# Kernel optimization log

Measured on AMD Instinct MI355X. Metric: run time of the kernel, lower is better.

The kernel has to match this reference:

```python
import jax, jax.numpy as jnp
import numpy as np

B, S, D_MODEL, D_HEAD = 4, 4096, 512, 64


def setup_inputs() -> dict:
    key = jax.random.key(0)
    ks = jax.random.split(key, 9)
    s = 1.0 / np.sqrt(D_MODEL)
    return {
        "q_in": jax.random.normal(ks[0], (B, S, D_MODEL), jnp.float32),
        "k_in": jax.random.normal(ks[1], (B, S, D_MODEL), jnp.float32),
        "v_in": jax.random.normal(ks[2], (B, S, D_MODEL), jnp.float32),
        "Wq": jax.random.normal(ks[3], (D_HEAD, D_MODEL), jnp.float32) * s,
        "bq": jax.random.normal(ks[4], (D_HEAD,), jnp.float32) * s,
        "Wk": jax.random.normal(ks[5], (D_HEAD, D_MODEL), jnp.float32) * s,
        "bk": jax.random.normal(ks[6], (D_HEAD,), jnp.float32) * s,
        "Wv": jax.random.normal(ks[7], (D_HEAD, D_MODEL), jnp.float32) * s,
        "bv": jax.random.normal(ks[8], (D_HEAD,), jnp.float32) * s,
    }


def reference(q_in, k_in, v_in, Wq, bq, Wk, bk, Wv, bv):
    # Linear projections (torch nn.Linear: x @ W.T + b)
    q = jnp.einsum("bsd,hd->bsh", q_in, Wq) + bq  # [B,S,Dh]
    k = jnp.einsum("bsd,hd->bsh", k_in, Wk) + bk
    v = jnp.einsum("bsd,hd->bsh", v_in, Wv) + bv
    # Causal mask: -inf strictly above diagonal (generate_attention_mask, triu(1))
    sk = k.shape[1]
    mask = jnp.triu(jnp.full((q.shape[1], sk), -jnp.inf, dtype=q.dtype), k=1)
    scores = jnp.einsum("bqh,bkh->bqk", q, k) / jnp.sqrt(jnp.asarray(q.shape[-1], q.dtype))
    attn = jax.nn.softmax(scores + mask, axis=-1)  # [B,S,S]
    return jnp.einsum("bqk,bkh->bqh", attn, v)
```

## Files before the change

### kernel.cpp

```cpp
#include <hip/hip_runtime.h>
#include <hip/hip_bf16.h>

#define B_ 4
#define S_ 4096
#define DM 512
#define DH 64

#define NEG_BIG (-3.0e38f)
#define MCLAMP  (-1.0e30f)

typedef __attribute__((ext_vector_type(8))) short short8b;
typedef __attribute__((ext_vector_type(4))) float f32x4;

__device__ __forceinline__ f32x4 MFMA16(short8b a, short8b b, f32x4 c) {
    return __builtin_amdgcn_mfma_f32_16x16x32_bf16(a, b, c, 0, 0, 0);
}

__device__ __forceinline__ float bf2f(unsigned short u) {
    unsigned int x = ((unsigned int)u) << 16;
    float f;
    __builtin_memcpy(&f, &x, 4);
    return f;
}
__device__ __forceinline__ unsigned short f2bf_rne(float f) {
    unsigned int u = __float_as_uint(f);
    u += 0x7FFFu + ((u >> 16) & 1u);
    return (unsigned short)(u >> 16);
}
__device__ __forceinline__ unsigned int pk2(unsigned short a, unsigned short b) {
    return (unsigned int)a | ((unsigned int)b << 16);
}

__device__ __forceinline__ void gload16(const void* gp, void* lp) {
    __builtin_amdgcn_global_load_lds(
        (const __attribute__((address_space(1))) void*)gp,
        (__attribute__((address_space(3))) void*)lp, 16, 0, 0);
}

__global__ void detect_kernel(const unsigned short* __restrict__ u,
                              int* __restrict__ flag) {
    __shared__ int cnt;
    if (threadIdx.x == 0) cnt = 0;
    __syncthreads();
    int w = 0;
    #pragma unroll
    for (int k = 0; k < 8; ++k) {
        unsigned short x = u[threadIdx.x * 8 + k];
        int e = (x >> 7) & 0xFF;
        if (e >= 135 || (e > 0 && e <= 95)) ++w;
    }
    atomicAdd(&cnt, w);
    __syncthreads();
    if (threadIdx.x == 0) *flag = (cnt > 64) ? 1 : 0;
}

#define PM 64
#define PK 64

__global__ __launch_bounds__(256) void proj_kernel(
    const void* __restrict__ xq, const void* __restrict__ xk,
    const void* __restrict__ xv,
    const void* __restrict__ Wq, const void* __restrict__ Wk,
    const void* __restrict__ Wv,
    const void* __restrict__ bq, const void* __restrict__ bk,
    const void* __restrict__ bv,
    unsigned short* __restrict__ Qhp, unsigned short* __restrict__ Qlp,
    unsigned short* __restrict__ Khp, unsigned short* __restrict__ Klp,
    unsigned short* __restrict__ Vthp, unsigned short* __restrict__ Vtlp,
    const int* __restrict__ flag)
{
    const int which = blockIdx.y;
    const void* x    = (which == 0) ? xq : (which == 1) ? xk : xv;
    const void* W    = (which == 0) ? Wq : (which == 1) ? Wk : Wv;
    const void* bias = (which == 0) ? bq : (which == 1) ? bk : bv;

    const bool f32 = (*flag != 0);
    const int row0 = blockIdx.x * PM;
    const int t    = threadIdx.x;
    const int lane = t & 63;
    const int w    = t >> 6;
    const int l15  = lane & 15;
    const int l4   = lane >> 4;

    __shared__ __align__(16) char sm[32768];

    const int srow = t >> 2;
    const int sseg = t & 3;
    const int swz  = (srow & 7) << 4;

    f32x4 acc[4];
    #pragma unroll
    for (int n = 0; n < 4; ++n) acc[n] = f32x4{0.f, 0.f, 0.f, 0.f};

    #pragma unroll 1
    for (int kc = 0; kc < DM / PK; ++kc) {
        const int k0 = kc * PK;
        __syncthreads();

        if (f32) {
            #pragma unroll
            for (int m = 0; m < 2; ++m) {
                const float* p = (m == 0)
                    ? (const float*)x + (size_t)(row0 + srow) * DM + k0 + sseg * 16
                    : (const float*)W + (size_t)srow * DM + k0 + sseg * 16;
                float v[16];
                #pragma unroll
                for (int j = 0; j < 4; ++j) {
                    float4 f = *reinterpret_cast<const float4*>(p + j * 4);
                    v[j * 4 + 0] = f.x; v[j * 4 + 1] = f.y;
                    v[j * 4 + 2] = f.z; v[j * 4 + 3] = f.w;
                }
                unsigned short hh[16], ll[16];
                #pragma unroll
                for (int j = 0; j < 16; ++j) {
                    unsigned short hb = f2bf_rne(v[j]);
                    hh[j] = hb;
                    ll[j] = f2bf_rne(v[j] - bf2f(hb));
                }
                char* dh = sm + m * 16384 + srow * 128;
                char* dl = dh + 8192;
                #pragma unroll
                for (int g = 0; g < 2; ++g) {
                    const int off = (sseg * 32 + g * 16) ^ swz;
                    uint4 hu, lu;
                    hu.x = pk2(hh[g*8+0], hh[g*8+1]); hu.y = pk2(hh[g*8+2], hh[g*8+3]);
                    hu.z = pk2(hh[g*8+4], hh[g*8+5]); hu.w = pk2(hh[g*8+6], hh[g*8+7]);
                    lu.x = pk2(ll[g*8+0], ll[g*8+1]); lu.y = pk2(ll[g*8+2], ll[g*8+3]);
                    lu.z = pk2(ll[g*8+4], ll[g*8+5]); lu.w = pk2(ll[g*8+6], ll[g*8+7]);
                    *reinterpret_cast<uint4*>(dh + off) = hu;
                    *reinterpret_cast<uint4*>(dl + off) = lu;
                }
            }
        } else {
            const uint4 z = {0u, 0u, 0u, 0u};
            #pragma unroll
            for (int m = 0; m < 2; ++m) {
                const unsigned short* p = (m == 0)
                    ? (const unsigned short*)x + (size_t)(row0 + srow) * DM + k0 + sseg * 16
                    : (const unsigned short*)W + (size_t)srow * DM + k0 + sseg * 16;
                char* dh = sm + m * 16384 + srow * 128;
                char* dl = dh + 8192;
                #pragma unroll
                for (int g = 0; g < 2; ++g) {
                    uint4 hv = *reinterpret_cast<const uint4*>(p + g * 8);
                    const int off = (sseg * 32 + g * 16) ^ swz;
                    *reinterpret_cast<uint4*>(dh + off) = hv;
                    *reinterpret_cast<uint4*>(dl + off) = z;
                }
            }
        }
        __syncthreads();

        const int arow = w * 16 + l15;
        short8b xh[2], xl[2];
        #pragma unroll
        for (int ks = 0; ks < 2; ++ks) {
            const int off = arow * 128 + ((ks * 64 + l4 * 16) ^ ((arow & 7) << 4));
            xh[ks] = *reinterpret_cast<const short8b*>(sm + off);
            xl[ks] = *reinterpret_cast<const short8b*>(sm + 8192 + off);
        }
        #pragma unroll
        for (int n = 0; n < 4; ++n) {
            #pragma unroll
            for (int ks = 0; ks < 2; ++ks) {
                const int brow = n * 16 + l15;
                const int off = brow * 128 + ((ks * 64 + l4 * 16) ^ ((brow & 7) << 4));
                short8b wh = *reinterpret_cast<const short8b*>(sm + 16384 + off);
                short8b wl = *reinterpret_cast<const short8b*>(sm + 24576 + off);
                acc[n] = MFMA16(xh[ks], wl, acc[n]);
                acc[n] = MFMA16(xl[ks], wh, acc[n]);
                acc[n] = MFMA16(xh[ks], wh, acc[n]);
            }
        }
    }

    __syncthreads();
    float* C = reinterpret_cast<float*>(sm);
    #pragma unroll
    for (int n = 0; n < 4; ++n)
        #pragma unroll
        for (int r = 0; r < 4; ++r)
            C[(w * 16 + l4 * 4 + r) * 66 + n * 16 + l15] = acc[n][r];
    __syncthreads();

    if (which < 2) {
        unsigned short* ph = (which == 0) ? Qhp : Khp;
        unsigned short* pl = (which == 0) ? Qlp : Klp;
        const float scale = (which == 0) ? 0.125f : 1.0f;
        const int r_  = t >> 2;
        const int c0_ = (t & 3) * 16;
        unsigned short hh[16], ll[16];
        #pragma unroll
        for (int j = 0; j < 16; ++j) {
            const float bv_ = f32 ? ((const float*)bias)[c0_ + j]
                                  : bf2f(((const unsigned short*)bias)[c0_ + j]);
            const float v = (C[r_ * 66 + c0_ + j] + bv_) * scale;
            unsigned short hb = f2bf_rne(v);
            hh[j] = hb;
            ll[j] = f2bf_rne(v - bf2f(hb));
        }
        const size_t off = (size_t)(row0 + r_) * DH + c0_;
        #pragma unroll
        for (int g = 0; g < 2; ++g) {
            uint4 hu, lu;
            hu.x = pk2(hh[g*8+0], hh[g*8+1]); hu.y = pk2(hh[g*8+2], hh[g*8+3]);
            hu.z = pk2(hh[g*8+4], hh[g*8+5]); hu.w = pk2(hh[g*8+6], hh[g*8+7]);
            lu.x = pk2(ll[g*8+0], ll[g*8+1]); lu.y = pk2(ll[g*8+2], ll[g*8+3]);
            lu.z = pk2(ll[g*8+4], ll[g*8+5]); lu.w = pk2(ll[g*8+6], ll[g*8+7]);
            *reinterpret_cast<uint4*>(ph + off + g * 8) = hu;
            *reinterpret_cast<uint4*>(pl + off + g * 8) = lu;
        }
    } else {
        const int c_ = t & 63;
        const int rb = (t >> 6) * 16;
        const int bb = row0 >> 12;
        const int s0 = row0 & (S_ - 1);
        const float bv_ = f32 ? ((const float*)bias)[c_]
                              : bf2f(((const unsigned short*)bias)[c_]);
        unsigned short hh[16], ll[16];
        #pragma unroll
        for (int i = 0; i < 16; ++i) {
            const float v = C[(rb + i) * 66 + c_] + bv_;
            unsigned short hb = f2bf_rne(v);
            hh[i] = hb;
            ll[i] = f2bf_rne(v - bf2f(hb));
        }
        const size_t off = (size_t)(bb * 64 + c_) * S_ + s0 + rb;
        #pragma unroll
        for (int g = 0; g < 2; ++g) {
            uint4 hu, lu;
            hu.x = pk2(hh[g*8+0], hh[g*8+1]); hu.y = pk2(hh[g*8+2], hh[g*8+3]);
            hu.z = pk2(hh[g*8+4], hh[g*8+5]); hu.w = pk2(hh[g*8+6], hh[g*8+7]);
            lu.x = pk2(ll[g*8+0], ll[g*8+1]); lu.y = pk2(ll[g*8+2], ll[g*8+3]);
            lu.z = pk2(ll[g*8+4], ll[g*8+5]); lu.w = pk2(ll[g*8+6], ll[g*8+7]);
            *reinterpret_cast<uint4*>(Vthp + off + g * 8) = hu;
            *reinterpret_cast<uint4*>(Vtlp + off + g * 8) = lu;
        }
    }
}

__global__ __launch_bounds__(512, 2) void flash_kernel(
    const unsigned short* __restrict__ Qh, const unsigned short* __restrict__ Ql,
    const unsigned short* __restrict__ Kh, const unsigned short* __restrict__ Kl,
    const unsigned short* __restrict__ Vth, const unsigned short* __restrict__ Vtl,
    void* __restrict__ out, const int* __restrict__ flag)
{
    const int pair = blockIdx.x;
    const int b    = blockIdx.y;
    const int t    = threadIdx.x;
    const int lane = t & 63;
    const int w    = t >> 6;
    const int qh   = w & 1;
    const int kh   = w >> 1;
    const int l15  = lane & 15;
    const int l4   = lane >> 4;

    __shared__ __align__(16) char smem[8192 + 2 * 65536];
    __shared__ float Mg[4][32];
    __shared__ float Lg[4][32];
    __shared__ float Ltot[32];

    const size_t bS = (size_t)b * S_;
    const bool f32o = (*flag != 0);

    const int qp   = t >> 8;
    const int qrow = (t & 255) >> 3;
    const int qsg  = t & 7;

    const int klaneoff = ((lane >> 3) << 7) +
                         ((((lane & 7) << 4)) ^ ((lane >> 3) << 4));
    const int vrl = lane >> 4;
    const int voff0 = (vrl << 13) + ((((lane & 15) << 4)) ^ (vrl << 4));
    const int voff1 = (vrl << 13) + ((((lane & 15) << 4)) ^ ((4 + vrl) << 4));

    const char* Khb = (const char*)Kh + bS * 128;
    const char* Klb = (const char*)Kl + bS * 128;
    const char* Vhb = (const char*)Vth + (size_t)b * 64 * 8192;
    const char* Vlb = (const char*)Vtl + (size_t)b * 64 * 8192;

    auto issue_tile = [&](int kt, int bsel) {
        char* buf = smem + 8192 + bsel * 65536;
        if (w < 4) {
            #pragma unroll
            for (int j = 0; j < 8; ++j) {
                const int c2  = w * 8 + j;
                const int p   = c2 >> 4;
                const int ckp = c2 & 15;
                const char* g = (p ? Klb : Khb) +
                                (size_t)kt * 16384 + ckp * 1024 + klaneoff;
                gload16(g, buf + p * 16384 + ckp * 1024);
            }
        } else {
            #pragma unroll
            for (int j = 0; j < 8; ++j) {
                const int c2  = (w - 4) * 8 + j;
                const int p   = c2 >> 4;
                const int cvp = c2 & 15;
                const int vo  = (cvp & 1) ? voff1 : voff0;
                const char* g = (p ? Vlb : Vhb) +
                                (size_t)cvp * 32768 + (size_t)kt * 256 + vo;
                gload16(g, buf + 32768 + p * 16384 + cvp * 1024);
            }
        }
    };

    #pragma unroll 1
    for (int hf = 0; hf < 2; ++hf) {
        const int qt = hf ? (127 - pair) : pair;
        const int q0 = qt << 5;
        const int nk = (qt >> 2) + 1;

        __syncthreads();

        {
            const unsigned short* src = qp ? Ql : Qh;
            uint4 v = *reinterpret_cast<const uint4*>(
                src + (bS + q0 + qrow) * 64 + qsg * 8);
            const int off = qp * 4096 + qrow * 128 +
                            ((qsg * 16) ^ ((qrow & 7) << 4));
            *reinterpret_cast<uint4*>(smem + off) = v;
        }
        issue_tile(0, 0);
        __syncthreads();

        short8b qf[2][2];
        #pragma unroll
        for (int p = 0; p < 2; ++p)
            #pragma unroll
            for (int ks = 0; ks < 2; ++ks) {
                const int row = qh * 16 + l15;
                const int off = p * 4096 + row * 128 +
                                ((ks * 64 + l4 * 16) ^ ((row & 7) << 4));
                qf[p][ks] = *reinterpret_cast<const short8b*>(smem + off);
            }
        __syncthreads();

        f32x4 of[4];
        of[0] = f32x4{0.f, 0.f, 0.f, 0.f};
        of[1] = f32x4{0.f, 0.f, 0.f, 0.f};
        of[2] = f32x4{0.f, 0.f, 0.f, 0.f};
        of[3] = f32x4{0.f, 0.f, 0.f, 0.f};
        float mrun[4], lrun[4];
        #pragma unroll
        for (int r = 0; r < 4; ++r) { mrun[r] = NEG_BIG; lrun[r] = 0.f; }

        #pragma unroll 1
        for (int kt = 0; kt < nk; ++kt) {
            const int bsel = kt & 1;
            if (kt + 1 < nk) issue_tile(kt + 1, bsel ^ 1);

            const char* kb = smem + 8192 + bsel * 65536;
            const char* vb = kb + 32768;

            f32x4 sc[2];
            #pragma unroll
            for (int ct = 0; ct < 2; ++ct) {
                f32x4 a = f32x4{0.f, 0.f, 0.f, 0.f};
                #pragma unroll
                for (int ks = 0; ks < 2; ++ks) {
                    const int row = kh * 32 + ct * 16 + l15;
                    const int off = row * 128 +
                                    ((ks * 64 + l4 * 16) ^ ((row & 7) << 4));
                    short8b bh = *reinterpret_cast<const short8b*>(kb + off);
                    short8b bl = *reinterpret_cast<const short8b*>(kb + 16384 + off);
                    a = MFMA16(qf[1][ks], bh, a);
                    a = MFMA16(qf[0][ks], bl, a);
                    a = MFMA16(qf[0][ks], bh, a);
                }
                sc[ct] = a;
            }

            if (kt == nk - 1) {
                #pragma unroll
                for (int ct = 0; ct < 2; ++ct) {
                    const int col = kt * 128 + kh * 32 + ct * 16 + l15;
                    #pragma unroll
                    for (int r = 0; r < 4; ++r) {
                        const int row = q0 + qh * 16 + l4 * 4 + r;
                        if (col > row) sc[ct][r] = NEG_BIG;
                    }
                }
            }

            float pm[4];
            #pragma unroll
            for (int r = 0; r < 4; ++r) pm[r] = fmaxf(sc[0][r], sc[1][r]);
            #pragma unroll
            for (int s = 1; s < 16; s <<= 1)
                #pragma unroll
                for (int r = 0; r < 4; ++r)
                    pm[r] = fmaxf(pm[r], __shfl_xor(pm[r], s));

            float alpha[4], ps[4];
            #pragma unroll
            for (int r = 0; r < 4; ++r) {
                const float mn = fmaxf(fmaxf(mrun[r], pm[r]), MCLAMP);
                alpha[r] = __expf(mrun[r] - mn);
                mrun[r] = mn;
                sc[0][r] = __expf(sc[0][r] - mn);
                sc[1][r] = __expf(sc[1][r] - mn);
                ps[r] = sc[0][r] + sc[1][r];
            }
            #pragma unroll
            for (int s = 1; s < 16; s <<= 1)
                #pragma unroll
                for (int r = 0; r < 4; ++r) ps[r] += __shfl_xor(ps[r], s);
            #pragma unroll
            for (int r = 0; r < 4; ++r) lrun[r] = lrun[r] * alpha[r] + ps[r];
            #pragma unroll
            for (int c = 0; c < 4; ++c)
                #pragma unroll
                for (int r = 0; r < 4; ++r) of[c][r] *= alpha[r];

            #pragma unroll
            for (int ct = 0; ct < 2; ++ct)
                #pragma unroll
                for (int r = 0; r < 4; ++r) {
                    const int row = qh * 16 + l4 * 4 + r;
                    const int col = kh * 32 + ct * 16 + l15;
                    const int off = row * 256 + ((col * 2) ^ ((row & 7) << 4));
                    *reinterpret_cast<unsigned short*>(smem + off) =
                        f2bf_rne(sc[ct][r]);
                }
            asm volatile("s_waitcnt lgkmcnt(0)" ::: "memory");
            __builtin_amdgcn_sched_barrier(0);

            short8b pf;
            {
                const int row = qh * 16 + l15;
                const int off = row * 256 + ((kh * 64 + l4 * 16) ^ ((row & 7) << 4));
                pf = *reinterpret_cast<const short8b*>(smem + off);
            }
            #pragma unroll
            for (int ct = 0; ct < 4; ++ct) {
                const int vr = ct * 16 + l15;
                const int voff = vr * 256 +
                                 ((kh * 64 + l4 * 16) ^ ((vr & 7) << 4));
                short8b vh = *reinterpret_cast<const short8b*>(vb + voff);
                short8b vl = *reinterpret_cast<const short8b*>(vb + 16384 + voff);
                of[ct] = MFMA16(pf, vl, of[ct]);
                of[ct] = MFMA16(pf, vh, of[ct]);
            }

            __syncthreads();
        }

        if (l15 == 0) {
            #pragma unroll
            for (int r = 0; r < 4; ++r) {
                const int row = qh * 16 + l4 * 4 + r;
                Mg[kh][row] = mrun[r];
                Lg[kh][row] = lrun[r];
            }
        }
        __syncthreads();

        float* Op = reinterpret_cast<float*>(smem + 8192);
        #pragma unroll
        for (int r = 0; r < 4; ++r) {
            const int row = qh * 16 + l4 * 4 + r;
            const float M = fmaxf(fmaxf(Mg[0][row], Mg[1][row]),
                                  fmaxf(Mg[2][row], Mg[3][row]));
            const float L = Lg[0][row] * __expf(Mg[0][row] - M)
                          + Lg[1][row] * __expf(Mg[1][row] - M)
                          + Lg[2][row] * __expf(Mg[2][row] - M)
                          + Lg[3][row] * __expf(Mg[3][row] - M);
            const float al = __expf(mrun[r] - M);
            #pragma unroll
            for (int c = 0; c < 4; ++c)
                Op[kh * 2048 + row * 64 + c * 16 + l15] = of[c][r] * al;
            if (kh == 0 && l15 == 0) Ltot[row] = L;
        }
        __syncthreads();

        {
            const int row = t >> 4;
            const int d0  = (t & 15) << 2;
            float4 s = {0.f, 0.f, 0.f, 0.f};
            #pragma unroll
            for (int g = 0; g < 4; ++g) {
                float4 v = *reinterpret_cast<const float4*>(
                    Op + g * 2048 + row * 64 + d0);
                s.x += v.x; s.y += v.y; s.z += v.z; s.w += v.w;
            }
            const float inv = 1.0f / Ltot[row];
            const size_t oi = (bS + q0 + row) * 64 + d0;
            if (f32o) {
                float4 o;
                o.x = s.x * inv; o.y = s.y * inv;
                o.z = s.z * inv; o.w = s.w * inv;
                *reinterpret_cast<float4*>((float*)out + oi) = o;
            } else {
                ushort4 o;
                o.x = f2bf_rne(s.x * inv);
                o.y = f2bf_rne(s.y * inv);
                o.z = f2bf_rne(s.z * inv);
                o.w = f2bf_rne(s.w * inv);
                *reinterpret_cast<ushort4*>((unsigned short*)out + oi) = o;
            }
        }
    }
}

extern "C" void kernel_launch(void* const* d_in, const int* in_sizes, int n_in,
                              void* d_out, int out_size, void* d_ws, size_t ws_size,
                              hipStream_t stream) {
    const size_t NP = (size_t)B_ * S_ * DH;
    unsigned short* Qhp  = (unsigned short*)d_ws;
    unsigned short* Qlp  = Qhp + NP;
    unsigned short* Khp  = Qhp + 2 * NP;
    unsigned short* Klp  = Qhp + 3 * NP;
    unsigned short* Vthp = Qhp + 4 * NP;
    unsigned short* Vtlp = Qhp + 5 * NP;
    int* flag = (int*)(Qhp + 6 * NP);

    detect_kernel<<<1, 256, 0, stream>>>((const unsigned short*)d_in[0], flag);

    proj_kernel<<<dim3(B_ * S_ / PM, 3), 256, 0, stream>>>(
        d_in[0], d_in[1], d_in[2],
        d_in[3], d_in[5], d_in[7],
        d_in[4], d_in[6], d_in[8],
        Qhp, Qlp, Khp, Klp, Vthp, Vtlp, flag);

    flash_kernel<<<dim3(64, B_), 512, 0, stream>>>(
        Qhp, Qlp, Khp, Klp, Vthp, Vtlp, d_out, flag);
}
```

Measured before the change: 220.0 us.

## Fuse detect, projection and flash attention into one cooperative persistent kernel

```diff
diff --git a/kernel.cpp b/kernel.cpp
--- a/kernel.cpp
+++ b/kernel.cpp
@@ -1,5 +1,8 @@
 #include <hip/hip_runtime.h>
 #include <hip/hip_bf16.h>
+#include <hip/hip_cooperative_groups.h>
+
+namespace cg = cooperative_groups;
 
 #define B_ 4
 #define S_ 4096
@@ -37,27 +40,7 @@
         (__attribute__((address_space(3))) void*)lp, 16, 0, 0);
 }
 
-__global__ void detect_kernel(const unsigned short* __restrict__ u,
-                              int* __restrict__ flag) {
-    __shared__ int cnt;
-    if (threadIdx.x == 0) cnt = 0;
-    __syncthreads();
-    int w = 0;
-    #pragma unroll
-    for (int k = 0; k < 8; ++k) {
-        unsigned short x = u[threadIdx.x * 8 + k];
-        int e = (x >> 7) & 0xFF;
-        if (e >= 135 || (e > 0 && e <= 95)) ++w;
-    }
-    atomicAdd(&cnt, w);
-    __syncthreads();
-    if (threadIdx.x == 0) *flag = (cnt > 64) ? 1 : 0;
-}
-
-#define PM 64
-#define PK 64
-
-__global__ __launch_bounds__(256) void proj_kernel(
+__global__ __launch_bounds__(512, 1) void fused_kernel(
     const void* __restrict__ xq, const void* __restrict__ xk,
     const void* __restrict__ xv,
     const void* __restrict__ Wq, const void* __restrict__ Wk,
@@ -67,436 +50,442 @@
     unsigned short* __restrict__ Qhp, unsigned short* __restrict__ Qlp,
     unsigned short* __restrict__ Khp, unsigned short* __restrict__ Klp,
     unsigned short* __restrict__ Vthp, unsigned short* __restrict__ Vtlp,
-    const int* __restrict__ flag)
+    void* __restrict__ out)
 {
-    const int which = blockIdx.y;
-    const void* x    = (which == 0) ? xq : (which == 1) ? xk : xv;
-    const void* W    = (which == 0) ? Wq : (which == 1) ? Wk : Wv;
-    const void* bias = (which == 0) ? bq : (which == 1) ? bk : bv;
-
-    const bool f32 = (*flag != 0);
-    const int row0 = blockIdx.x * PM;
+    const int blk  = blockIdx.x;
     const int t    = threadIdx.x;
     const int lane = t & 63;
     const int w    = t >> 6;
     const int l15  = lane & 15;
     const int l4   = lane >> 4;
 
-    __shared__ __align__(16) char sm[32768];
-
-    const int srow = t >> 2;
-    const int sseg = t & 3;
-    const int swz  = (srow & 7) << 4;
-
-    f32x4 acc[4];
-    #pragma unroll
-    for (int n = 0; n < 4; ++n) acc[n] = f32x4{0.f, 0.f, 0.f, 0.f};
-
-    #pragma unroll 1
-    for (int kc = 0; kc < DM / PK; ++kc) {
-        const int k0 = kc * PK;
-        __syncthreads();
-
-        if (f32) {
-            #pragma unroll
-            for (int m = 0; m < 2; ++m) {
-                const float* p = (m == 0)
-                    ? (const float*)x + (size_t)(row0 + srow) * DM + k0 + sseg * 16
-                    : (const float*)W + (size_t)srow * DM + k0 + sseg * 16;
-                float v[16];
-                #pragma unroll
-                for (int j = 0; j < 4; ++j) {
-                    float4 f = *reinterpret_cast<const float4*>(p + j * 4);
-                    v[j * 4 + 0] = f.x; v[j * 4 + 1] = f.y;
-                    v[j * 4 + 2] = f.z; v[j * 4 + 3] = f.w;
-                }
-                unsigned short hh[16], ll[16];
-                #pragma unroll
-                for (int j = 0; j < 16; ++j) {
-                    unsigned short hb = f2bf_rne(v[j]);
-                    hh[j] = hb;
-                    ll[j] = f2bf_rne(v[j] - bf2f(hb));
-                }
-                char* dh = sm + m * 16384 + srow * 128;
-                char* dl = dh + 8192;
-                #pragma unroll
-                for (int g = 0; g < 2; ++g) {
-                    const int off = (sseg * 32 + g * 16) ^ swz;
-                    uint4 hu, lu;
-                    hu.x = pk2(hh[g*8+0], hh[g*8+1]); hu.y = pk2(hh[g*8+2], hh[g*8+3]);
-                    hu.z = pk2(hh[g*8+4], hh[g*8+5]); hu.w = pk2(hh[g*8+6], hh[g*8+7]);
-                    lu.x = pk2(ll[g*8+0], ll[g*8+1]); lu.y = pk2(ll[g*8+2], ll[g*8+3]);
-                    lu.z = pk2(ll[g*8+4], ll[g*8+5]); lu.w = pk2(ll[g*8+6], ll[g*8+7]);
-                    *reinterpret_cast<uint4*>(dh + off) = hu;
-                    *reinterpret_cast<uint4*>(dl + off) = lu;
-                }
-            }
-        } else {
-            const uint4 z = {0u, 0u, 0u, 0u};
-            #pragma unroll
-            for (int m = 0; m < 2; ++m) {
-                const unsigned short* p = (m == 0)
-                    ? (const unsigned short*)x + (size_t)(row0 + srow) * DM + k0 + sseg * 16
-                    : (const unsigned short*)W + (size_t)srow * DM + k0 + sseg * 16;
-                char* dh = sm + m * 16384 + srow * 128;
-                char* dl = dh + 8192;
-                #pragma unroll
-                for (int g = 0; g < 2; ++g) {
-                    uint4 hv = *reinterpret_cast<const uint4*>(p + g * 8);
-                    const int off = (sseg * 32 + g * 16) ^ swz;
-                    *reinterpret_cast<uint4*>(dh + off) = hv;
-                    *reinterpret_cast<uint4*>(dl + off) = z;
-                }
-            }
-        }
-        __syncthreads();
-
-        const int arow = w * 16 + l15;
-        short8b xh[2], xl[2];
-        #pragma unroll
-        for (int ks = 0; ks < 2; ++ks) {
-            const int off = arow * 128 + ((ks * 64 + l4 * 16) ^ ((arow & 7) << 4));
-            xh[ks] = *reinterpret_cast<const short8b*>(sm + off);
-            xl[ks] = *reinterpret_cast<const short8b*>(sm + 8192 + off);
-        }
-        #pragma unroll
-        for (int n = 0; n < 4; ++n) {
-            #pragma unroll
-            for (int ks = 0; ks < 2; ++ks) {
-                const int brow = n * 16 + l15;
-                const int off = brow * 128 + ((ks * 64 + l4 * 16) ^ ((brow & 7) << 4));
-                short8b wh = *reinterpret_cast<const short8b*>(sm + 16384 + off);
-                short8b wl = *reinterpret_cast<const short8b*>(sm + 24576 + off);
-                acc[n] = MFMA16(xh[ks], wl, acc[n]);
-                acc[n] = MFMA16(xl[ks], wh, acc[n]);
-                acc[n] = MFMA16(xh[ks], wh, acc[n]);
-            }
-        }
-    }
-
-    __syncthreads();
-    float* C = reinterpret_cast<float*>(sm);
-    #pragma unroll
-    for (int n = 0; n < 4; ++n)
-        #pragma unroll
-        for (int r = 0; r < 4; ++r)
-            C[(w * 16 + l4 * 4 + r) * 66 + n * 16 + l15] = acc[n][r];
-    __syncthreads();
-
-    if (which < 2) {
-        unsigned short* ph = (which == 0) ? Qhp : Khp;
-        unsigned short* pl = (which == 0) ? Qlp : Klp;
-        const float scale = (which == 0) ? 0.125f : 1.0f;
-        const int r_  = t >> 2;
-        const int c0_ = (t & 3) * 16;
-        unsigned short hh[16], ll[16];
-        #pragma unroll
-        for (int j = 0; j < 16; ++j) {
-            const float bv_ = f32 ? ((const float*)bias)[c0_ + j]
-                                  : bf2f(((const unsigned short*)bias)[c0_ + j]);
-            const float v = (C[r_ * 66 + c0_ + j] + bv_) * scale;
-            unsigned short hb = f2bf_rne(v);
-            hh[j] = hb;
-            ll[j] = f2bf_rne(v - bf2f(hb));
-        }
-        const size_t off = (size_t)(row0 + r_) * DH + c0_;
-        #pragma unroll
-        for (int g = 0; g < 2; ++g) {
-            uint4 hu, lu;
-            hu.x = pk2(hh[g*8+0], hh[g*8+1]); hu.y = pk2(hh[g*8+2], hh[g*8+3]);
-            hu.z = pk2(hh[g*8+4], hh[g*8+5]); hu.w = pk2(hh[g*8+6], hh[g*8+7]);
-            lu.x = pk2(ll[g*8+0], ll[g*8+1]); lu.y = pk2(ll[g*8+2], ll[g*8+3]);
-            lu.z = pk2(ll[g*8+4], ll[g*8+5]); lu.w = pk2(ll[g*8+6], ll[g*8+7]);
-            *reinterpret_cast<uint4*>(ph + off + g * 8) = hu;
-            *reinterpret_cast<uint4*>(pl + off + g * 8) = lu;
-        }
-    } else {
-        const int c_ = t & 63;
-        const int rb = (t >> 6) * 16;
-        const int bb = row0 >> 12;
-        const int s0 = row0 & (S_ - 1);
-        const float bv_ = f32 ? ((const float*)bias)[c_]
-                              : bf2f(((const unsigned short*)bias)[c_]);
-        unsigned short hh[16], ll[16];
-        #pragma unroll
-        for (int i = 0; i < 16; ++i) {
-            const float v = C[(rb + i) * 66 + c_] + bv_;
-            unsigned short hb = f2bf_rne(v);
-            hh[i] = hb;
-            ll[i] = f2bf_rne(v - bf2f(hb));
-        }
-        const size_t off = (size_t)(bb * 64 + c_) * S_ + s0 + rb;
-        #pragma unroll
-        for (int g = 0; g < 2; ++g) {
-            uint4 hu, lu;
-            hu.x = pk2(hh[g*8+0], hh[g*8+1]); hu.y = pk2(hh[g*8+2], hh[g*8+3]);
-            hu.z = pk2(hh[g*8+4], hh[g*8+5]); hu.w = pk2(hh[g*8+6], hh[g*8+7]);
-            lu.x = pk2(ll[g*8+0], ll[g*8+1]); lu.y = pk2(ll[g*8+2], ll[g*8+3]);
-            lu.z = pk2(ll[g*8+4], ll[g*8+5]); lu.w = pk2(ll[g*8+6], ll[g*8+7]);
-            *reinterpret_cast<uint4*>(Vthp + off + g * 8) = hu;
-            *reinterpret_cast<uint4*>(Vtlp + off + g * 8) = lu;
-        }
-    }
-}
-
-__global__ __launch_bounds__(512, 2) void flash_kernel(
-    const unsigned short* __restrict__ Qh, const unsigned short* __restrict__ Ql,
-    const unsigned short* __restrict__ Kh, const unsigned short* __restrict__ Kl,
-    const unsigned short* __restrict__ Vth, const unsigned short* __restrict__ Vtl,
-    void* __restrict__ out, const int* __restrict__ flag)
-{
-    const int pair = blockIdx.x;
-    const int b    = blockIdx.y;
-    const int t    = threadIdx.x;
-    const int lane = t & 63;
-    const int w    = t >> 6;
-    const int qh   = w & 1;
-    const int kh   = w >> 1;
-    const int l15  = lane & 15;
-    const int l4   = lane >> 4;
-
     __shared__ __align__(16) char smem[8192 + 2 * 65536];
     __shared__ float Mg[4][32];
     __shared__ float Lg[4][32];
     __shared__ float Ltot[32];
-
-    const size_t bS = (size_t)b * S_;
-    const bool f32o = (*flag != 0);
-
-    const int qp   = t >> 8;
-    const int qrow = (t & 255) >> 3;
-    const int qsg  = t & 7;
-
-    const int klaneoff = ((lane >> 3) << 7) +
-                         ((((lane & 7) << 4)) ^ ((lane >> 3) << 4));
-    const int vrl = lane >> 4;
-    const int voff0 = (vrl << 13) + ((((lane & 15) << 4)) ^ (vrl << 4));
-    const int voff1 = (vrl << 13) + ((((lane & 15) << 4)) ^ ((4 + vrl) << 4));
-
-    const char* Khb = (const char*)Kh + bS * 128;
-    const char* Klb = (const char*)Kl + bS * 128;
-    const char* Vhb = (const char*)Vth + (size_t)b * 64 * 8192;
-    const char* Vlb = (const char*)Vtl + (size_t)b * 64 * 8192;
-
-    auto issue_tile = [&](int kt, int bsel) {
-        char* buf = smem + 8192 + bsel * 65536;
-        if (w < 4) {
+    __shared__ int sdet;
+
+    if (t == 0) sdet = 0;
+    __syncthreads();
+    if (t < 256) {
+        const unsigned short* u = (const unsigned short*)xq;
+        int cnt = 0;
+        #pragma unroll
+        for (int k = 0; k < 8; ++k) {
+            unsigned short x = u[t * 8 + k];
+            int e = (x >> 7) & 0xFF;
+            if (e >= 135 || (e > 0 && e <= 95)) ++cnt;
+        }
+        atomicAdd(&sdet, cnt);
+    }
+    __syncthreads();
+    const bool f32 = (sdet > 64);
+
+    {
+        const int row0 = blk * 64;
+        const int m    = t >> 8;
+        const int tt   = t & 255;
+        const int srow = tt >> 2;
+        const int sseg = tt & 3;
+        const int swz  = (srow & 7) << 4;
+        const int rq   = (w & 3) * 16;
+        const int nb   = (w >> 2) * 2;
+        const int arow = rq + l15;
+
+        #pragma unroll 1
+        for (int which = 0; which < 3; ++which) {
+            const void* x    = (which == 0) ? xq : (which == 1) ? xk : xv;
+            const void* W    = (which == 0) ? Wq : (which == 1) ? Wk : Wv;
+            const void* bias = (which == 0) ? bq : (which == 1) ? bk : bv;
+
+            f32x4 acc[2];
+            acc[0] = f32x4{0.f, 0.f, 0.f, 0.f};
+            acc[1] = f32x4{0.f, 0.f, 0.f, 0.f};
+
+            #pragma unroll 1
+            for (int kc = 0; kc < DM / 64; ++kc) {
+                const int k0 = kc * 64;
+                __syncthreads();
+
+                if (f32) {
+                    const float* p = (m == 0)
+                        ? (const float*)x + (size_t)(row0 + srow) * DM + k0 + sseg * 16
+                        : (const float*)W + (size_t)srow * DM + k0 + sseg * 16;
+                    float v[16];
+                    #pragma unroll
+                    for (int j = 0; j < 4; ++j) {
+                        float4 f = *reinterpret_cast<const float4*>(p + j * 4);
+                        v[j*4+0] = f.x; v[j*4+1] = f.y;
+                        v[j*4+2] = f.z; v[j*4+3] = f.w;
+                    }
+                    unsigned short hh[16], ll[16];
+                    #pragma unroll
+                    for (int j = 0; j < 16; ++j) {
+                        unsigned short hb = f2bf_rne(v[j]);
+                        hh[j] = hb;
+                        ll[j] = f2bf_rne(v[j] - bf2f(hb));
+                    }
+                    char* dh = smem + m * 16384 + srow * 128;
+                    char* dl = dh + 8192;
+                    #pragma unroll
+                    for (int g = 0; g < 2; ++g) {
+                        const int off = (sseg * 32 + g * 16) ^ swz;
+                        uint4 hu, lu;
+                        hu.x = pk2(hh[g*8+0], hh[g*8+1]); hu.y = pk2(hh[g*8+2], hh[g*8+3]);
+                        hu.z = pk2(hh[g*8+4], hh[g*8+5]); hu.w = pk2(hh[g*8+6], hh[g*8+7]);
+                        lu.x = pk2(ll[g*8+0], ll[g*8+1]); lu.y = pk2(ll[g*8+2], ll[g*8+3]);
+                        lu.z = pk2(ll[g*8+4], ll[g*8+5]); lu.w = pk2(ll[g*8+6], ll[g*8+7]);
+                        *reinterpret_cast<uint4*>(dh + off) = hu;
+                        *reinterpret_cast<uint4*>(dl + off) = lu;
+                    }
+                } else {
+                    const unsigned short* p = (m == 0)
+                        ? (const unsigned short*)x + (size_t)(row0 + srow) * DM + k0 + sseg * 16
+                        : (const unsigned short*)W + (size_t)srow * DM + k0 + sseg * 16;
+                    char* dh = smem + m * 16384 + srow * 128;
+                    char* dl = dh + 8192;
+                    const uint4 z = {0u, 0u, 0u, 0u};
+                    #pragma unroll
+                    for (int g = 0; g < 2; ++g) {
+                        uint4 hv = *reinterpret_cast<const uint4*>(p + g * 8);
+                        const int off = (sseg * 32 + g * 16) ^ swz;
+                        *reinterpret_cast<uint4*>(dh + off) = hv;
+                        *reinterpret_cast<uint4*>(dl + off) = z;
+                    }
+                }
+                __syncthreads();
+
+                short8b xh[2], xl[2];
+                #pragma unroll
+                for (int ks = 0; ks < 2; ++ks) {
+                    const int off = arow * 128 + ((ks * 64 + l4 * 16) ^ ((arow & 7) << 4));
+                    xh[ks] = *reinterpret_cast<const short8b*>(smem + off);
+                    xl[ks] = *reinterpret_cast<const short8b*>(smem + 8192 + off);
+                }
+                #pragma unroll
+                for (int n2 = 0; n2 < 2; ++n2) {
+                    const int brow = (nb + n2) * 16 + l15;
+                    #pragma unroll
+                    for (int ks = 0; ks < 2; ++ks) {
+                        const int off = brow * 128 + ((ks * 64 + l4 * 16) ^ ((brow & 7) << 4));
+                        short8b wh = *reinterpret_cast<const short8b*>(smem + 16384 + off);
+                        short8b wl = *reinterpret_cast<const short8b*>(smem + 24576 + off);
+                        acc[n2] = MFMA16(xh[ks], wl, acc[n2]);
+                        acc[n2] = MFMA16(xl[ks], wh, acc[n2]);
+                        acc[n2] = MFMA16(xh[ks], wh, acc[n2]);
+                    }
+                }
+            }
+
+            __syncthreads();
+            float* C = reinterpret_cast<float*>(smem + 32768);
             #pragma unroll
-            for (int j = 0; j < 8; ++j) {
-                const int c2  = w * 8 + j;
-                const int p   = c2 >> 4;
-                const int ckp = c2 & 15;
-                const char* g = (p ? Klb : Khb) +
-                                (size_t)kt * 16384 + ckp * 1024 + klaneoff;
-                gload16(g, buf + p * 16384 + ckp * 1024);
-            }
-        } else {
+            for (int n2 = 0; n2 < 2; ++n2)
+                #pragma unroll
+                for (int r = 0; r < 4; ++r)
+                    C[(rq + l4 * 4 + r) * 66 + (nb + n2) * 16 + l15] = acc[n2][r];
+            __syncthreads();
+
+            if (which < 2) {
+                unsigned short* ph = (which == 0) ? Qhp : Khp;
+                unsigned short* pl = (which == 0) ? Qlp : Klp;
+                const float scale = (which == 0) ? 0.125f : 1.0f;
+                const int r_  = t >> 3;
+                const int c0_ = (t & 7) * 8;
+                unsigned short hh[8], ll[8];
+                #pragma unroll
+                for (int j = 0; j < 8; ++j) {
+                    const float bv_ = f32 ? ((const float*)bias)[c0_ + j]
+                                          : bf2f(((const unsigned short*)bias)[c0_ + j]);
+                    const float v = (C[r_ * 66 + c0_ + j] + bv_) * scale;
+                    unsigned short hb = f2bf_rne(v);
+                    hh[j] = hb;
+                    ll[j] = f2bf_rne(v - bf2f(hb));
+                }
+                const size_t off = (size_t)(row0 + r_) * DH + c0_;
+                uint4 hu, lu;
+                hu.x = pk2(hh[0], hh[1]); hu.y = pk2(hh[2], hh[3]);
+                hu.z = pk2(hh[4], hh[5]); hu.w = pk2(hh[6], hh[7]);
+                lu.x = pk2(ll[0], ll[1]); lu.y = pk2(ll[2], ll[3]);
+                lu.z = pk2(ll[4], ll[5]); lu.w = pk2(ll[6], ll[7]);
+                *reinterpret_cast<uint4*>(ph + off) = hu;
+                *reinterpret_cast<uint4*>(pl + off) = lu;
+            } else {
+                const int c_ = t & 63;
+                const int rb = (t >> 6) * 8;
+                const int bb = row0 >> 12;
+                const int s0 = row0 & (S_ - 1);
+                const float bv_ = f32 ? ((const float*)bias)[c_]
+                                      : bf2f(((const unsigned short*)bias)[c_]);
+                unsigned short hh[8], ll[8];
+                #pragma unroll
+                for (int i = 0; i < 8; ++i) {
+                    const float v = C[(rb + i) * 66 + c_] + bv_;
+                    unsigned short hb = f2bf_rne(v);
+                    hh[i] = hb;
+                    ll[i] = f2bf_rne(v - bf2f(hb));
+                }
+                const size_t off = (size_t)(bb * 64 + c_) * S_ + s0 + rb;
+                uint4 hu, lu;
+                hu.x = pk2(hh[0], hh[1]); hu.y = pk2(hh[2], hh[3]);
+                hu.z = pk2(hh[4], hh[5]); hu.w = pk2(hh[6], hh[7]);
+                lu.x = pk2(ll[0], ll[1]); lu.y = pk2(ll[2], ll[3]);
+                lu.z = pk2(ll[4], ll[5]); lu.w = pk2(ll[6], ll[7]);
+                *reinterpret_cast<uint4*>(Vthp + off) = hu;
+                *reinterpret_cast<uint4*>(Vtlp + off) = lu;
+            }
+        }
+    }
+
+    __threadfence();
+    cg::this_grid().sync();
+
+    {
+        const int pair = blk & 63;
+        const int b    = blk >> 6;
+        const int qh   = w & 1;
+        const int kh   = w >> 1;
+
+        const size_t bS = (size_t)b * S_;
+        const bool f32o = f32;
+
+        const int qp   = t >> 8;
+        const int qrow = (t & 255) >> 3;
+        const int qsg  = t & 7;
+
+        const int klaneoff = ((lane >> 3) << 7) +
+                             ((((lane & 7) << 4)) ^ ((lane >> 3) << 4));
+        const int vrl = lane >> 4;
+        const int voff0 = (vrl << 13) + ((((lane & 15) << 4)) ^ (vrl << 4));
+        const int voff1 = (vrl << 13) + ((((lane & 15) << 4)) ^ ((4 + vrl) << 4));
+
+        const char* Khb = (const char*)Khp + bS * 128;
+        const char* Klb = (const char*)Klp + bS * 128;
+        const char* Vhb = (const char*)Vthp + (size_t)b * 64 * 8192;
+        const char* Vlb = (const char*)Vtlp + (size_t)b * 64 * 8192;
+
+        auto issue_tile = [&](int kt, int bsel) {
+            char* buf = smem + 8192 + bsel * 65536;
+            if (w < 4) {
+                #pragma unroll
+                for (int j = 0; j < 8; ++j) {
+                    const int c2  = w * 8 + j;
+                    const int p   = c2 >> 4;
+                    const int ckp = c2 & 15;
+                    const char* g = (p ? Klb : Khb) +
+                                    (size_t)kt * 16384 + ckp * 1024 + klaneoff;
+                    gload16(g, buf + p * 16384 + ckp * 1024);
+                }
+            } else {
+                #pragma unroll
+                for (int j = 0; j < 8; ++j) {
+                    const int c2  = (w - 4) * 8 + j;
+                    const int p   = c2 >> 4;
+                    const int cvp = c2 & 15;
+                    const int vo  = (cvp & 1) ? voff1 : voff0;
+                    const char* g = (p ? Vlb : Vhb) +
+                                    (size_t)cvp * 32768 + (size_t)kt * 256 + vo;
+                    gload16(g, buf + 32768 + p * 16384 + cvp * 1024);
+                }
+            }
+        };
+
+        #pragma unroll 1
+        for (int hf = 0; hf < 2; ++hf) {
+            const int qt = hf ? (127 - pair) : pair;
+            const int q0 = qt << 5;
+            const int nk = (qt >> 2) + 1;
+
+            __syncthreads();
+
+            {
+                const unsigned short* src = qp ? Qlp : Qhp;
+                uint4 v = *reinterpret_cast<const uint4*>(
+                    src + (bS + q0 + qrow) * 64 + qsg * 8);
+                const int off = qp * 4096 + qrow * 128 +
+                                ((qsg * 16) ^ ((qrow & 7) << 4));
+                *reinterpret_cast<uint4*>(smem + off) = v;
+            }
+            issue_tile(0, 0);
+            __syncthreads();
+
+            short8b qf[2][2];
             #pragma unroll
-            for (int j = 0; j < 8; ++j) {
-                const int c2  = (w - 4) * 8 + j;
-                const int p   = c2 >> 4;
-                const int cvp = c2 & 15;
-                const int vo  = (cvp & 1) ? voff1 : voff0;
-                const char* g = (p ? Vlb : Vhb) +
-                                (size_t)cvp * 32768 + (size_t)kt * 256 + vo;
-                gload16(g, buf + 32768 + p * 16384 + cvp * 1024);
-            }
-        }
-    };
-
-    #pragma unroll 1
-    for (int hf = 0; hf < 2; ++hf) {
-        const int qt = hf ? (127 - pair) : pair;
-        const int q0 = qt << 5;
-        const int nk = (qt >> 2) + 1;
-
-        __syncthreads();
-
-        {
-            const unsigned short* src = qp ? Ql : Qh;
-            uint4 v = *reinterpret_cast<const uint4*>(
-                src + (bS + q0 + qrow) * 64 + qsg * 8);
-            const int off = qp * 4096 + qrow * 128 +
-                            ((qsg * 16) ^ ((qrow & 7) << 4));
-            *reinterpret_cast<uint4*>(smem + off) = v;
-        }
-        issue_tile(0, 0);
-        __syncthreads();
-
-        short8b qf[2][2];
-        #pragma unroll
-        for (int p = 0; p < 2; ++p)
+            for (int p = 0; p < 2; ++p)
+                #pragma unroll
+                for (int ks = 0; ks < 2; ++ks) {
+                    const int row = qh * 16 + l15;
+                    const int off = p * 4096 + row * 128 +
+                                    ((ks * 64 + l4 * 16) ^ ((row & 7) << 4));
+                    qf[p][ks] = *reinterpret_cast<const short8b*>(smem + off);
+                }
+            __syncthreads();
+
+            f32x4 of[4];
+            of[0] = f32x4{0.f, 0.f, 0.f, 0.f};
+            of[1] = f32x4{0.f, 0.f, 0.f, 0.f};
+            of[2] = f32x4{0.f, 0.f, 0.f, 0.f};
+            of[3] = f32x4{0.f, 0.f, 0.f, 0.f};
+            float mrun[4], lrun[4];
             #pragma unroll
-            for (int ks = 0; ks < 2; ++ks) {
-                const int row = qh * 16 + l15;
-                const int off = p * 4096 + row * 128 +
-                                ((ks * 64 + l4 * 16) ^ ((row & 7) << 4));
-                qf[p][ks] = *reinterpret_cast<const short8b*>(smem + off);
-            }
-        __syncthreads();
-
-        f32x4 of[4];
-        of[0] = f32x4{0.f, 0.f, 0.f, 0.f};
-        of[1] = f32x4{0.f, 0.f, 0.f, 0.f};
-        of[2] = f32x4{0.f, 0.f, 0.f, 0.f};
-        of[3] = f32x4{0.f, 0.f, 0.f, 0.f};
-        float mrun[4], lrun[4];
-        #pragma unroll
-        for (int r = 0; r < 4; ++r) { mrun[r] = NEG_BIG; lrun[r] = 0.f; }
-
-        #pragma unroll 1
-        for (int kt = 0; kt < nk; ++kt) {
-            const int bsel = kt & 1;
-            if (kt + 1 < nk) issue_tile(kt + 1, bsel ^ 1);
-
-            const char* kb = smem + 8192 + bsel * 65536;
-            const char* vb = kb + 32768;
-
-            f32x4 sc[2];
-            #pragma unroll
-            for (int ct = 0; ct < 2; ++ct) {
-                f32x4 a = f32x4{0.f, 0.f, 0.f, 0.f};
-                #pragma unroll
-                for (int ks = 0; ks < 2; ++ks) {
-                    const int row = kh * 32 + ct * 16 + l15;
-                    const int off = row * 128 +
-                                    ((ks * 64 + l4 * 16) ^ ((row & 7) << 4));
-                    short8b bh = *reinterpret_cast<const short8b*>(kb + off);
-                    short8b bl = *reinterpret_cast<const short8b*>(kb + 16384 + off);
-                    a = MFMA16(qf[1][ks], bh, a);
-                    a = MFMA16(qf[0][ks], bl, a);
-                    a = MFMA16(qf[0][ks], bh, a);
-                }
-                sc[ct] = a;
-            }
-
-            if (kt == nk - 1) {
+            for (int r = 0; r < 4; ++r) { mrun[r] = NEG_BIG; lrun[r] = 0.f; }
+
+            #pragma unroll 1
+            for (int kt = 0; kt < nk; ++kt) {
+                const int bsel = kt & 1;
+                if (kt + 1 < nk) issue_tile(kt + 1, bsel ^ 1);
+
+                const char* kb = smem + 8192 + bsel * 65536;
+                const char* vb = kb + 32768;
+
+                f32x4 sc[2];
                 #pragma unroll
                 for (int ct = 0; ct < 2; ++ct) {
-                    const int col = kt * 128 + kh * 32 + ct * 16 + l15;
+                    f32x4 a = f32x4{0.f, 0.f, 0.f, 0.f};
+                    #pragma unroll
+                    for (int ks = 0; ks < 2; ++ks) {
+                        const int row = kh * 32 + ct * 16 + l15;
+                        const int off = row * 128 +
+                                        ((ks * 64 + l4 * 16) ^ ((row & 7) << 4));
+                        short8b bh = *reinterpret_cast<const short8b*>(kb + off);
+                        short8b bl = *reinterpret_cast<const short8b*>(kb + 16384 + off);
+                        a = MFMA16(qf[1][ks], bh, a);
+                        a = MFMA16(qf[0][ks], bl, a);
+                        a = MFMA16(qf[0][ks], bh, a);
+                    }
+                    sc[ct] = a;
+                }
+
+                if (kt == nk - 1) {
+                    #pragma unroll
+                    for (int ct = 0; ct < 2; ++ct) {
+                        const int col = kt * 128 + kh * 32 + ct * 16 + l15;
+                        #pragma unroll
+                        for (int r = 0; r < 4; ++r) {
+                            const int row = q0 + qh * 16 + l4 * 4 + r;
+                            if (col > row) sc[ct][r] = NEG_BIG;
+                        }
+                    }
+                }
+
+                float pm[4];
+                #pragma unroll
+                for (int r = 0; r < 4; ++r) pm[r] = fmaxf(sc[0][r], sc[1][r]);
+                #pragma unroll
+                for (int s = 1; s < 16; s <<= 1)
+                    #pragma unroll
+                    for (int r = 0; r < 4; ++r)
+                        pm[r] = fmaxf(pm[r], __shfl_xor(pm[r], s));
+
+                float alpha[4], ps[4];
+                #pragma unroll
+                for (int r = 0; r < 4; ++r) {
+                    const float mn = fmaxf(fmaxf(mrun[r], pm[r]), MCLAMP);
+                    alpha[r] = __expf(mrun[r] - mn);
+                    mrun[r] = mn;
+                    sc[0][r] = __expf(sc[0][r] - mn);
+                    sc[1][r] = __expf(sc[1][r] - mn);
+                    ps[r] = sc[0][r] + sc[1][r];
+                }
+                #pragma unroll
+                for (int s = 1; s < 16; s <<= 1)
+                    #pragma unroll
+                    for (int r = 0; r < 4; ++r) ps[r] += __shfl_xor(ps[r], s);
+                #pragma unroll
+                for (int r = 0; r < 4; ++r) lrun[r] = lrun[r] * alpha[r] + ps[r];
+                #pragma unroll
+                for (int c = 0; c < 4; ++c)
+                    #pragma unroll
+                    for (int r = 0; r < 4; ++r) of[c][r] *= alpha[r];
+
+                #pragma unroll
+                for (int ct = 0; ct < 2; ++ct)
                     #pragma unroll
                     for (int r = 0; r < 4; ++r) {
-                        const int row = q0 + qh * 16 + l4 * 4 + r;
-                        if (col > row) sc[ct][r] = NEG_BIG;
-                    }
-                }
-            }
-
-            float pm[4];
-            #pragma unroll
-            for (int r = 0; r < 4; ++r) pm[r] = fmaxf(sc[0][r], sc[1][r]);
-            #pragma unroll
-            for (int s = 1; s < 16; s <<= 1)
-                #pragma unroll
-                for (int r = 0; r < 4; ++r)
-                    pm[r] = fmaxf(pm[r], __shfl_xor(pm[r], s));
-
-            float alpha[4], ps[4];
-            #pragma unroll
-            for (int r = 0; r < 4; ++r) {
-                const float mn = fmaxf(fmaxf(mrun[r], pm[r]), MCLAMP);
-                alpha[r] = __expf(mrun[r] - mn);
-                mrun[r] = mn;
-                sc[0][r] = __expf(sc[0][r] - mn);
-                sc[1][r] = __expf(sc[1][r] - mn);
-                ps[r] = sc[0][r] + sc[1][r];
-            }
-            #pragma unroll
-            for (int s = 1; s < 16; s <<= 1)
-                #pragma unroll
-                for (int r = 0; r < 4; ++r) ps[r] += __shfl_xor(ps[r], s);
-            #pragma unroll
-            for (int r = 0; r < 4; ++r) lrun[r] = lrun[r] * alpha[r] + ps[r];
-            #pragma unroll
-            for (int c = 0; c < 4; ++c)
-                #pragma unroll
-                for (int r = 0; r < 4; ++r) of[c][r] *= alpha[r];
-
-            #pragma unroll
-            for (int ct = 0; ct < 2; ++ct)
+                        const int row = qh * 16 + l4 * 4 + r;
+                        const int col = kh * 32 + ct * 16 + l15;
+                        const int off = row * 256 + ((col * 2) ^ ((row & 7) << 4));
+                        *reinterpret_cast<unsigned short*>(smem + off) =
+                            f2bf_rne(sc[ct][r]);
+                    }
+                asm volatile("s_waitcnt lgkmcnt(0)" ::: "memory");
+                __builtin_amdgcn_sched_barrier(0);
+
+                short8b pf;
+                {
+                    const int row = qh * 16 + l15;
+                    const int off = row * 256 + ((kh * 64 + l4 * 16) ^ ((row & 7) << 4));
+                    pf = *reinterpret_cast<const short8b*>(smem + off);
+                }
+                #pragma unroll
+                for (int ct = 0; ct < 4; ++ct) {
+                    const int vr = ct * 16 + l15;
+                    const int voff = vr * 256 +
+                                     ((kh * 64 + l4 * 16) ^ ((vr & 7) << 4));
+                    short8b vh = *reinterpret_cast<const short8b*>(vb + voff);
+                    short8b vl = *reinterpret_cast<const short8b*>(vb + 16384 + voff);
+                    of[ct] = MFMA16(pf, vl, of[ct]);
+                    of[ct] = MFMA16(pf, vh, of[ct]);
+                }
+
+                __syncthreads();
+            }
+
+            if (l15 == 0) {
                 #pragma unroll
                 for (int r = 0; r < 4; ++r) {
                     const int row = qh * 16 + l4 * 4 + r;
-                    const int col = kh * 32 + ct * 16 + l15;
-                    const int off = row * 256 + ((col * 2) ^ ((row & 7) << 4));
-                    *reinterpret_cast<unsigned short*>(smem + off) =
-                        f2bf_rne(sc[ct][r]);
-                }
-            asm volatile("s_waitcnt lgkmcnt(0)" ::: "memory");
-            __builtin_amdgcn_sched_barrier(0);
-
-            short8b pf;
-            {
-                const int row = qh * 16 + l15;
-                const int off = row * 256 + ((kh * 64 + l4 * 16) ^ ((row & 7) << 4));
-                pf = *reinterpret_cast<const short8b*>(smem + off);
-            }
-            #pragma unroll
-            for (int ct = 0; ct < 4; ++ct) {
-                const int vr = ct * 16 + l15;
-                const int voff = vr * 256 +
-                                 ((kh * 64 + l4 * 16) ^ ((vr & 7) << 4));
-                short8b vh = *reinterpret_cast<const short8b*>(vb + voff);
-                short8b vl = *reinterpret_cast<const short8b*>(vb + 16384 + voff);
-                of[ct] = MFMA16(pf, vl, of[ct]);
-                of[ct] = MFMA16(pf, vh, of[ct]);
-            }
-
-            __syncthreads();
-        }
-
-        if (l15 == 0) {
+                    Mg[kh][row] = mrun[r];
+                    Lg[kh][row] = lrun[r];
+                }
+            }
+            __syncthreads();
+
+            float* Op = reinterpret_cast<float*>(smem + 8192);
             #pragma unroll
             for (int r = 0; r < 4; ++r) {
                 const int row = qh * 16 + l4 * 4 + r;
-                Mg[kh][row] = mrun[r];
-                Lg[kh][row] = lrun[r];
-            }
-        }
-        __syncthreads();
-
-        float* Op = reinterpret_cast<float*>(smem + 8192);
-        #pragma unroll
-        for (int r = 0; r < 4; ++r) {
-            const int row = qh * 16 + l4 * 4 + r;
-            const float M = fmaxf(fmaxf(Mg[0][row], Mg[1][row]),
-                                  fmaxf(Mg[2][row], Mg[3][row]));
-            const float L = Lg[0][row] * __expf(Mg[0][row] - M)
-                          + Lg[1][row] * __expf(Mg[1][row] - M)
-                          + Lg[2][row] * __expf(Mg[2][row] - M)
-                          + Lg[3][row] * __expf(Mg[3][row] - M);
-            const float al = __expf(mrun[r] - M);
-            #pragma unroll
-            for (int c = 0; c < 4; ++c)
-                Op[kh * 2048 + row * 64 + c * 16 + l15] = of[c][r] * al;
-            if (kh == 0 && l15 == 0) Ltot[row] = L;
-        }
-        __syncthreads();
-
-        {
-            const int row = t >> 4;
-            const int d0  = (t & 15) << 2;
-            float4 s = {0.f, 0.f, 0.f, 0.f};
-            #pragma unroll
-            for (int g = 0; g < 4; ++g) {
-                float4 v = *reinterpret_cast<const float4*>(
-                    Op + g * 2048 + row * 64 + d0);
-                s.x += v.x; s.y += v.y; s.z += v.z; s.w += v.w;
-            }
-            const float inv = 1.0f / Ltot[row];
-            const size_t oi = (bS + q0 + row) * 64 + d0;
-            if (f32o) {
-                float4 o;
-                o.x = s.x * inv; o.y = s.y * inv;
-                o.z = s.z * inv; o.w = s.w * inv;
-                *reinterpret_cast<float4*>((float*)out + oi) = o;
-            } else {
-                ushort4 o;
-                o.x = f2bf_rne(s.x * inv);
-                o.y = f2bf_rne(s.y * inv);
-                o.z = f2bf_rne(s.z * inv);
-                o.w = f2bf_rne(s.w * inv);
-                *reinterpret_cast<ushort4*>((unsigned short*)out + oi) = o;
+                const float M = fmaxf(fmaxf(Mg[0][row], Mg[1][row]),
+                                      fmaxf(Mg[2][row], Mg[3][row]));
+                const float L = Lg[0][row] * __expf(Mg[0][row] - M)
+                              + Lg[1][row] * __expf(Mg[1][row] - M)
+                              + Lg[2][row] * __expf(Mg[2][row] - M)
+                              + Lg[3][row] * __expf(Mg[3][row] - M);
+                const float al = __expf(mrun[r] - M);
+                #pragma unroll
+                for (int c = 0; c < 4; ++c)
+                    Op[kh * 2048 + row * 64 + c * 16 + l15] = of[c][r] * al;
+                if (kh == 0 && l15 == 0) Ltot[row] = L;
+            }
+            __syncthreads();
+
+            {
+                const int row = (t >> 4) & 31;
+                const int d0  = (t & 15) << 2;
+                float4 s = {0.f, 0.f, 0.f, 0.f};
+                #pragma unroll
+                for (int g = 0; g < 4; ++g) {
+                    float4 v = *reinterpret_cast<const float4*>(
+                        Op + g * 2048 + row * 64 + d0);
+                    s.x += v.x; s.y += v.y; s.z += v.z; s.w += v.w;
+                }
+                const float inv = 1.0f / Ltot[row];
+                const size_t oi = (bS + q0 + row) * 64 + d0;
+                if (t < 512) {
+                    if (f32o) {
+                        float4 o;
+                        o.x = s.x * inv; o.y = s.y * inv;
+                        o.z = s.z * inv; o.w = s.w * inv;
+                        *reinterpret_cast<float4*>((float*)out + oi) = o;
+                    } else {
+                        ushort4 o;
+                        o.x = f2bf_rne(s.x * inv);
+                        o.y = f2bf_rne(s.y * inv);
+                        o.z = f2bf_rne(s.z * inv);
+                        o.w = f2bf_rne(s.w * inv);
+                        *reinterpret_cast<ushort4*>((unsigned short*)out + oi) = o;
+                    }
+                }
             }
         }
     }
@@ -512,16 +501,20 @@
     unsigned short* Klp  = Qhp + 3 * NP;
     unsigned short* Vthp = Qhp + 4 * NP;
     unsigned short* Vtlp = Qhp + 5 * NP;
-    int* flag = (int*)(Qhp + 6 * NP);
-
-    detect_kernel<<<1, 256, 0, stream>>>((const unsigned short*)d_in[0], flag);
-
-    proj_kernel<<<dim3(B_ * S_ / PM, 3), 256, 0, stream>>>(
-        d_in[0], d_in[1], d_in[2],
-        d_in[3], d_in[5], d_in[7],
-        d_in[4], d_in[6], d_in[8],
-        Qhp, Qlp, Khp, Klp, Vthp, Vtlp, flag);
-
-    flash_kernel<<<dim3(64, B_), 512, 0, stream>>>(
-        Qhp, Qlp, Khp, Klp, Vthp, Vtlp, d_out, flag);
-}
+
+    const void* xq = d_in[0]; const void* xk = d_in[1]; const void* xv = d_in[2];
+    const void* Wq = d_in[3]; const void* bq = d_in[4];
+    const void* Wk = d_in[5]; const void* bk = d_in[6];
+    const void* Wv = d_in[7]; const void* bv = d_in[8];
+    void* outp = d_out;
+
+    void* args[] = {
+        (void*)&xq, (void*)&xk, (void*)&xv,
+        (void*)&Wq, (void*)&Wk, (void*)&Wv,
+        (void*)&bq, (void*)&bk, (void*)&bv,
+        (void*)&Qhp, (void*)&Qlp, (void*)&Khp, (void*)&Klp,
+        (void*)&Vthp, (void*)&Vtlp, (void*)&outp
+    };
+    hipLaunchCooperativeKernel((void*)fused_kernel, dim3(256), dim3(512),
+                               args, 0, stream);
+}
```

Result: slower. 351.6 us (+59.8%).
